# Optimization experiments

Measured on AMD Instinct MI355X. Metric: run time of the kernel, lower is better.

Reference implementation:

```python
import jax, jax.numpy as jnp
import numpy as np

B, S, E = 1, 2048, 2048
H, G, HD = 16, 4, 128  # heads, kv groups, head_dim; out_dim = H*HD = 2048
OUT_DIM = H * HD


def _rope_tables(seq_len, head_dim, base=10000.0):
    # Standard RoPE tables, full head_dim width (matches apply_rope's cos[:seq_len, :] of shape [S, HD])
    inv_freq = 1.0 / (base ** (np.arange(0, head_dim, 2, dtype=np.float32) / head_dim))
    t = np.arange(seq_len, dtype=np.float32)
    ang = np.outer(t, inv_freq)                      # [S, HD/2]
    ang = np.concatenate([ang, ang], axis=-1)        # [S, HD]
    return jnp.asarray(np.cos(ang)), jnp.asarray(np.sin(ang))


def setup_inputs() -> dict:
    key = jax.random.key(0)
    ks = jax.random.split(key, 6)
    x = jax.random.normal(ks[0], (B, S, E), dtype=jnp.float32)
    # causal mask: True above the diagonal => masked out (torch.triu(..., diagonal=1))
    mask = jnp.triu(jnp.ones((S, S), dtype=bool), k=1)
    cos, sin = _rope_tables(S, HD)
    scale = 0.02
    Wq = jax.random.normal(ks[1], (E, H * HD), dtype=jnp.float32) * scale
    Wk = jax.random.normal(ks[2], (E, G * HD), dtype=jnp.float32) * scale
    Wv = jax.random.normal(ks[3], (E, G * HD), dtype=jnp.float32) * scale
    Wout = jax.random.normal(ks[4], (H * HD, OUT_DIM), dtype=jnp.float32) * scale
    return {"x": x, "mask": mask, "cos": cos, "sin": sin,
            "Wq": Wq, "Wk": Wk, "Wv": Wv, "Wout": Wout}


def _apply_rope(t, cos, sin):
    # t: [B, h, S, HD]; cos/sin: [S, HD]
    hd = t.shape[-1]
    x1, x2 = t[..., : hd // 2], t[..., hd // 2 :]
    rotated = jnp.concatenate((-x2, x1), axis=-1)
    return t * cos[None, None] + rotated * sin[None, None]


def reference(x, mask, cos, sin, Wq, Wk, Wv, Wout):
    b, s, _ = x.shape
    q = (x @ Wq).reshape(b, s, H, HD).transpose(0, 2, 1, 3)   # [B,H,S,HD]
    k = (x @ Wk).reshape(b, s, G, HD).transpose(0, 2, 1, 3)   # [B,G,S,HD]
    v = (x @ Wv).reshape(b, s, G, HD).transpose(0, 2, 1, 3)
    q = _apply_rope(q, cos, sin)
    k = _apply_rope(k, cos, sin)
    rep = H // G
    k = jnp.repeat(k, rep, axis=1)                            # [B,H,S,HD]
    v = jnp.repeat(v, rep, axis=1)
    scores = jnp.einsum("bhqd,bhkd->bhqk", q, k)              # [B,H,S,S]
    scores = jnp.where(mask[None, None], -jnp.inf, scores)
    p = jax.nn.softmax(scores / jnp.sqrt(jnp.float32(HD)), axis=-1)
    o = jnp.einsum("bhqk,bhkd->bhqd", p, v)                   # [B,H,S,HD]
    o = o.transpose(0, 2, 1, 3).reshape(b, s, OUT_DIM)
    return (o @ Wout, p)
```

## Files before the change

### kernel.cpp

```cpp
#include <hip/hip_runtime.h>
#include <stdint.h>

#define S 2048
#define E 2048
#define NH 16
#define NG 4
#define HD 128
#define BK 64

using short8 = __attribute__((ext_vector_type(8))) short;
using f32x4  = __attribute__((ext_vector_type(4))) float;

__device__ __forceinline__ unsigned short f2bf(float f){
    union { float f; unsigned int i; } v; v.f = f;
    unsigned int x = v.i;
    unsigned int r = x + 0x7FFFu + ((x >> 16) & 1u);
    return (unsigned short)(r >> 16);
}

__device__ __forceinline__ void async_cp16(const unsigned short* g, unsigned short* l){
    __builtin_amdgcn_global_load_lds((const __attribute__((address_space(1))) void*)g,
                                     (__attribute__((address_space(3))) void*)l,
                                     16, 0, 0);
}

__device__ __forceinline__ void stage_tile_async(const unsigned short* __restrict__ G,
                                                 int ld, int k0,
                                                 unsigned short* lds)
{
    int tid = threadIdx.x;
    #pragma unroll
    for (int c = 0; c < 4; c++) {
        int e  = (c * 256 + tid) * 8;
        int r  = e >> 6;
        int cl = (e >> 3) & 7;
        int sc = cl ^ (r & 7);
        async_cp16(G + (size_t)r * ld + k0 + sc * 8, lds + e);
    }
}

__device__ __forceinline__ void stage_128x128(const unsigned short* __restrict__ G,
                                              int ld, unsigned short* lds)
{
    int tid = threadIdx.x;
    #pragma unroll
    for (int c = 0; c < 8; c++) {
        int e  = (c * 256 + tid) * 8;
        int r  = e >> 7;
        int cl = (e >> 3) & 15;
        int sc = cl ^ (r & 15);
        async_cp16(G + (size_t)r * ld + sc * 8, lds + e);
    }
}

__device__ __forceinline__ void stage_64x128(const unsigned short* __restrict__ G,
                                             int ld, unsigned short* lds)
{
    int tid = threadIdx.x;
    #pragma unroll
    for (int c = 0; c < 4; c++) {
        int e  = (c * 256 + tid) * 8;
        int r  = e >> 7;
        int cl = (e >> 3) & 15;
        int sc = cl ^ (r & 15);
        async_cp16(G + (size_t)r * ld + sc * 8, lds + e);
    }
}

__device__ __forceinline__ void gemm_core_async(const unsigned short* __restrict__ A, int lda,
                                                const unsigned short* __restrict__ Bt, int ldb,
                                                int K, f32x4 acc[4][4],
                                                unsigned short* lA, unsigned short* lB)
{
    int tid = threadIdx.x;
    int wave = tid >> 6, lane = tid & 63;
    int mBase = (wave >> 1) * 64, nBase = (wave & 1) * 64;
    int rowA = lane & 15, qc = lane >> 4;
    for (int k0 = 0; k0 < K; k0 += BK) {
        __syncthreads();
        stage_tile_async(A,  lda, k0, lA);
        stage_tile_async(Bt, ldb, k0, lB);
        __syncthreads();
        #pragma unroll
        for (int s = 0; s < 2; s++) {
            short8 af[4], bfr[4];
            #pragma unroll
            for (int i = 0; i < 4; i++) {
                int r  = mBase + i * 16 + rowA;
                int ch = (s * 4 + qc) ^ (r & 7);
                af[i] = *(const short8*)&lA[r * BK + ch * 8];
            }
            #pragma unroll
            for (int j = 0; j < 4; j++) {
                int r  = nBase + j * 16 + rowA;
                int ch = (s * 4 + qc) ^ (r & 7);
                bfr[j] = *(const short8*)&lB[r * BK + ch * 8];
            }
            #pragma unroll
            for (int i = 0; i < 4; i++)
                #pragma unroll
                for (int j = 0; j < 4; j++)
                    acc[i][j] = __builtin_amdgcn_mfma_f32_16x16x32_bf16(af[i], bfr[j], acc[i][j], 0, 0, 0);
        }
    }
}

template<bool BF16OUT>
__device__ __forceinline__ void epilogue(f32x4 acc[4][4], void* Cv, int ldc,
                                         int row0, int col0, float scale)
{
    int tid = threadIdx.x, wave = tid >> 6, lane = tid & 63;
    int mBase = (wave >> 1) * 64, nBase = (wave & 1) * 64;
    int col = lane & 15, quad = lane >> 4;
    #pragma unroll
    for (int i = 0; i < 4; i++)
        #pragma unroll
        for (int j = 0; j < 4; j++)
            #pragma unroll
            for (int r = 0; r < 4; r++) {
                int gr = row0 + mBase + i * 16 + quad * 4 + r;
                int gc = col0 + nBase + j * 16 + col;
                float v = acc[i][j][r] * scale;
                if (BF16OUT) ((unsigned short*)Cv)[(size_t)gr * ldc + gc] = f2bf(v);
                else         ((float*)Cv)[(size_t)gr * ldc + gc] = v;
            }
}

template<bool BF16OUT>
__global__ __launch_bounds__(256) void gemm_mfma_as(const unsigned short* __restrict__ A, int lda,
                                                    const unsigned short* __restrict__ Bt, int ldb,
                                                    void* __restrict__ C, int ldc, int K)
{
    __shared__ unsigned short lA[128 * BK];
    __shared__ unsigned short lB[128 * BK];
    int row0 = blockIdx.y * 128, col0 = blockIdx.x * 128;
    f32x4 acc[4][4] = {};
    gemm_core_async(A + (size_t)row0 * lda, lda, Bt + (size_t)col0 * ldb, ldb, K, acc, lA, lB);
    epilogue<BF16OUT>(acc, C, ldc, row0, col0, 1.0f);
}

__device__ __forceinline__ float rmax16(float v){
    v = fmaxf(v, __shfl_xor(v, 1)); v = fmaxf(v, __shfl_xor(v, 2));
    v = fmaxf(v, __shfl_xor(v, 4)); v = fmaxf(v, __shfl_xor(v, 8));
    return v;
}
__device__ __forceinline__ float rsum16(float v){
    v += __shfl_xor(v, 1); v += __shfl_xor(v, 2);
    v += __shfl_xor(v, 4); v += __shfl_xor(v, 8);
    return v;
}

__device__ __forceinline__ void qk_compute(const short8 qf[4], const unsigned short* lK,
                                           int rowA, int quad, f32x4 sacc[8])
{
    #pragma unroll
    for (int j = 0; j < 8; j++)
        #pragma unroll
        for (int r = 0; r < 4; r++) sacc[j][r] = 0.f;
    #pragma unroll
    for (int ks = 0; ks < 4; ks++) {
        int ch = (ks * 4 + quad) ^ rowA;
        #pragma unroll
        for (int j = 0; j < 8; j++) {
            short8 kf = *(const short8*)&lK[(j * 16 + rowA) * 128 + ch * 8];
            sacc[j] = __builtin_amdgcn_mfma_f32_16x16x32_bf16(qf[ks], kf, sacc[j], 0, 0, 0);
        }
    }
}

__global__ __launch_bounds__(256, 2) void attn_fused(const unsigned short* __restrict__ Q,
                                                     const unsigned short* __restrict__ Kb,
                                                     const unsigned short* __restrict__ Vt,
                                                     float* __restrict__ P,
                                                     unsigned short* __restrict__ Obf)
{
    __shared__ unsigned short lK[128 * 128];
    __shared__ unsigned short lV[128 * 128];
    __shared__ unsigned short lP[64 * 128];
    int h = blockIdx.x, qt = blockIdx.y, g = h >> 2;
    int jtm = qt >> 1;
    int rbase = (qt & 1) * 64;
    int tid = threadIdx.x, wave = tid >> 6, lane = tid & 63;
    int rowA = lane & 15, quad = lane >> 4;

    stage_64x128(Q + (size_t)(qt * 64) * (NH * HD) + h * HD, NH * HD, lK);
    __syncthreads();
    short8 qf[4];
    #pragma unroll
    for (int ks = 0; ks < 4; ks++) {
        int r = wave * 16 + rowA;
        int ch = (ks * 4 + quad) ^ rowA;
        qf[ks] = *(const short8*)&lK[r * 128 + ch * 8];
    }

    f32x4 m_, l_;
    #pragma unroll
    for (int r = 0; r < 4; r++) { m_[r] = -1e30f; l_[r] = 0.f; }

    for (int jt = 0; jt <= jtm; ++jt) {
        __syncthreads();
        stage_128x128(Kb + (size_t)(jt * 128) * (NG * HD) + g * HD, NG * HD, lK);
        __syncthreads();
        f32x4 sacc[8];
        qk_compute(qf, lK, rowA, quad, sacc);
        if (jt == jtm) {
            #pragma unroll
            for (int j = 0; j < 8; j++)
                #pragma unroll
                for (int r = 0; r < 4; r++) {
                    int row = rbase + wave * 16 + quad * 4 + r;
                    int col = j * 16 + rowA;
                    if (col > row) sacc[j][r] = -1e30f;
                }
        }
        #pragma unroll
        for (int r = 0; r < 4; r++) {
            float tm = sacc[0][r];
            #pragma unroll
            for (int j = 1; j < 8; j++) tm = fmaxf(tm, sacc[j][r]);
            tm = rmax16(tm);
            float mn = fmaxf(m_[r], tm);
            float es = 0.f;
            #pragma unroll
            for (int j = 0; j < 8; j++) es += __expf(sacc[j][r] - mn);
            es = rsum16(es);
            l_[r] = l_[r] * __expf(m_[r] - mn) + es;
            m_[r] = mn;
        }
    }
    f32x4 linv;
    #pragma unroll
    for (int r = 0; r < 4; r++) linv[r] = 1.0f / l_[r];

    f32x4 oacc[8];
    #pragma unroll
    for (int j = 0; j < 8; j++)
        #pragma unroll
        for (int r = 0; r < 4; r++) oacc[j][r] = 0.f;

    for (int jt = 0; jt <= jtm; ++jt) {
        __syncthreads();
        stage_128x128(Kb + (size_t)(jt * 128) * (NG * HD) + g * HD, NG * HD, lK);
        stage_128x128(Vt + (size_t)(g * HD) * S + jt * 128, S, lV);
        __syncthreads();
        f32x4 sacc[8];
        qk_compute(qf, lK, rowA, quad, sacc);
        if (jt == jtm) {
            #pragma unroll
            for (int j = 0; j < 8; j++)
                #pragma unroll
                for (int r = 0; r < 4; r++) {
                    int row = rbase + wave * 16 + quad * 4 + r;
                    int col = j * 16 + rowA;
                    if (col > row) sacc[j][r] = -1e30f;
                }
        }
        float* Prow = P + ((size_t)h * S + qt * 64) * S + jt * 128;
        #pragma unroll
        for (int j = 0; j < 8; j++)
            #pragma unroll
            for (int r = 0; r < 4; r++) {
                int row = wave * 16 + quad * 4 + r;
                int col = j * 16 + rowA;
                float pv = __expf(sacc[j][r] - m_[r]) * linv[r];
                Prow[(size_t)row * S + col] = pv;
                int ch = col >> 3;
                lP[row * 128 + (((ch ^ (row & 15)) << 3) | (col & 7))] = f2bf(pv);
            }
        __syncthreads();
        #pragma unroll
        for (int ks = 0; ks < 4; ks++) {
            int ch = (ks * 4 + quad) ^ rowA;
            short8 pa = *(const short8*)&lP[(wave * 16 + rowA) * 128 + ch * 8];
            #pragma unroll
            for (int j = 0; j < 8; j++) {
                short8 vb = *(const short8*)&lV[(j * 16 + rowA) * 128 + ch * 8];
                oacc[j] = __builtin_amdgcn_mfma_f32_16x16x32_bf16(pa, vb, oacc[j], 0, 0, 0);
            }
        }
    }

    #pragma unroll
    for (int j = 0; j < 8; j++)
        #pragma unroll
        for (int r = 0; r < 4; r++) {
            int row = qt * 64 + wave * 16 + quad * 4 + r;
            int col = h * HD + j * 16 + rowA;
            Obf[(size_t)row * (NH * HD) + col] = f2bf(oacc[j][r]);
        }

    int zc0 = (jtm + 1) * 128;
    float* Pz = P + ((size_t)h * S + qt * 64) * S;
    for (int rr = 0; rr < 64; ++rr)
        for (int c = zc0 + tid * 4; c < S; c += 1024)
            *(float4*)(Pz + (size_t)rr * S + c) = make_float4(0.f, 0.f, 0.f, 0.f);
}

__global__ __launch_bounds__(256) void transpose_cvt(const float* __restrict__ in,
                                                     unsigned short* __restrict__ out,
                                                     int R, int C, int inLd)
{
    __shared__ float t[32][33];
    int r0 = blockIdx.y * 32, c0 = blockIdx.x * 32;
    int tid = threadIdx.x;
    int rr = tid >> 3, cc = (tid & 7) * 4;
    float4 v = *(const float4*)(in + (size_t)(r0 + rr) * inLd + c0 + cc);
    t[rr][cc] = v.x; t[rr][cc + 1] = v.y; t[rr][cc + 2] = v.z; t[rr][cc + 3] = v.w;
    __syncthreads();
    int oc = tid >> 3, orr = (tid & 7) * 4;
    ushort4 o;
    o.x = f2bf(t[orr][oc]);     o.y = f2bf(t[orr + 1][oc]);
    o.z = f2bf(t[orr + 2][oc]); o.w = f2bf(t[orr + 3][oc]);
    *(ushort4*)(out + (size_t)(c0 + oc) * R + r0 + orr) = o;
}

__global__ __launch_bounds__(256) void cvt_bf16(const float* __restrict__ in,
                                                unsigned short* __restrict__ out, int n)
{
    int i = (blockIdx.x * 256 + threadIdx.x) * 8;
    if (i >= n) return;
    float4 a = *(const float4*)(in + i);
    float4 b = *(const float4*)(in + i + 4);
    unsigned int w0 = (unsigned int)f2bf(a.x) | ((unsigned int)f2bf(a.y) << 16);
    unsigned int w1 = (unsigned int)f2bf(a.z) | ((unsigned int)f2bf(a.w) << 16);
    unsigned int w2 = (unsigned int)f2bf(b.x) | ((unsigned int)f2bf(b.y) << 16);
    unsigned int w3 = (unsigned int)f2bf(b.z) | ((unsigned int)f2bf(b.w) << 16);
    *(uint4*)(out + i) = make_uint4(w0, w1, w2, w3);
}

__global__ void rope_bf16(const float* __restrict__ T, unsigned short* __restrict__ Tb,
                          const float* __restrict__ cosp, const float* __restrict__ sinp,
                          int nHeads, int inLd, int inOff, int outLd, float scale, int total)
{
    int idx = blockIdx.x * blockDim.x + threadIdx.x;
    if (idx >= total) return;
    int d = idx & 63;
    int head = (idx >> 6) % nHeads;
    int s = idx / (nHeads * 64);
    float c  = cosp[s * HD + d];
    float sn = sinp[s * HD + d];
    const float* ib = T + (size_t)s * inLd + inOff + head * HD + d;
    float x1 = ib[0], x2 = ib[64];
    unsigned short* ob = Tb + (size_t)s * outLd + head * HD + d;
    ob[0]  = f2bf((x1 * c - x2 * sn) * scale);
    ob[64] = f2bf((x2 * c + x1 * sn) * scale);
}

extern "C" void kernel_launch(void* const* d_in, const int* in_sizes, int n_in,
                              void* d_out, int out_size, void* d_ws, size_t ws_size,
                              hipStream_t stream)
{
    const float* x    = (const float*)d_in[0];
    const float* cosp = (const float*)d_in[2];
    const float* sinp = (const float*)d_in[3];
    const float* Wq   = (const float*)d_in[4];
    const float* Wk   = (const float*)d_in[5];
    const float* Wv   = (const float*)d_in[6];
    const float* Wout = (const float*)d_in[7];

    float* out0 = (float*)d_out;
    float* Pout = out0 + (size_t)S * E;

    unsigned short* Wqkvt = (unsigned short*)d_ws;
    unsigned short* Qbf   = Wqkvt + (size_t)3072 * E;
    unsigned short* Kbf   = Qbf   + (size_t)S * E;
    unsigned short* Vt    = Kbf   + (size_t)S * (NG * HD);
    unsigned short* Obf   = Vt    + (size_t)(NG * HD) * S;
    float* QKVb = (float*)(Obf + (size_t)S * E);
    unsigned short* xbf   = Obf;
    unsigned short* Woutt = (unsigned short*)QKVb;

    dim3 blk(256);
    transpose_cvt<<<dim3(E / 32, E / 32), blk, 0, stream>>>(Wq, Wqkvt, E, E, E);
    transpose_cvt<<<dim3((NG * HD) / 32, E / 32), blk, 0, stream>>>(Wk, Wqkvt + (size_t)E * E, E, NG * HD, NG * HD);
    transpose_cvt<<<dim3((NG * HD) / 32, E / 32), blk, 0, stream>>>(Wv, Wqkvt + (size_t)(E + NG * HD) * E, E, NG * HD, NG * HD);
    cvt_bf16<<<dim3((S * E) / (256 * 8)), blk, 0, stream>>>(x, xbf, S * E);

    gemm_mfma_as<false><<<dim3(3072 / 128, S / 128), blk, 0, stream>>>(xbf, E, Wqkvt, E, QKVb, 3072, E);

    rope_bf16<<<(S * NH * 64 + 255) / 256, blk, 0, stream>>>(QKVb, Qbf, cosp, sinp, NH, 3072, 0, NH * HD,
                                                             0.08838834764831845f, S * NH * 64);
    rope_bf16<<<(S * NG * 64 + 255) / 256, blk, 0, stream>>>(QKVb, Kbf, cosp, sinp, NG, 3072, E, NG * HD,
                                                             1.0f, S * NG * 64);
    transpose_cvt<<<dim3((NG * HD) / 32, S / 32), blk, 0, stream>>>(QKVb + E + NG * HD, Vt, S, NG * HD, 3072);

    transpose_cvt<<<dim3(E / 32, E / 32), blk, 0, stream>>>(Wout, Woutt, E, E, E);

    attn_fused<<<dim3(NH, S / 64), blk, 0, stream>>>(Qbf, Kbf, Vt, Pout, Obf);

    gemm_mfma_as<false><<<dim3(E / 128, S / 128), blk, 0, stream>>>(Obf, E, Woutt, E, out0, E, E);
}
```

Before: 498.9 us.

## Split attention into single-pass flash kernel plus separate tiled P writer

Replaces the two-pass attention (a stats pass, then recompute and write P) with a one-pass online-softmax flash kernel that saves only the row max and inverse sum. A new p_write kernel recomputes QK^T per 128x128 tile using those stats and writes the normalized probabilities or zeros with coalesced, well-parallelized stores. The GEMM core also gains double-buffered LDS staging to overlap loads with MFMA, and attention blocks are launched in reverse order so the longest causal rows start first. This costs an extra QK^T recompute and doubles GEMM shared memory.

```diff
diff --git a/kernel.cpp b/kernel.cpp
--- a/kernel.cpp
+++ b/kernel.cpp
@@ -76,11 +76,18 @@
     int wave = tid >> 6, lane = tid & 63;
     int mBase = (wave >> 1) * 64, nBase = (wave & 1) * 64;
     int rowA = lane & 15, qc = lane >> 4;
-    for (int k0 = 0; k0 < K; k0 += BK) {
-        __syncthreads();
-        stage_tile_async(A,  lda, k0, lA);
-        stage_tile_async(Bt, ldb, k0, lB);
-        __syncthreads();
+    int nt = K / BK;
+    stage_tile_async(A,  lda, 0, lA);
+    stage_tile_async(Bt, ldb, 0, lB);
+    __syncthreads();
+    int cur = 0;
+    for (int t = 0; t < nt; ++t) {
+        if (t + 1 < nt) {
+            stage_tile_async(A,  lda, (t + 1) * BK, lA + (cur ^ 1) * (128 * BK));
+            stage_tile_async(Bt, ldb, (t + 1) * BK, lB + (cur ^ 1) * (128 * BK));
+        }
+        const unsigned short* cA = lA + cur * (128 * BK);
+        const unsigned short* cB = lB + cur * (128 * BK);
         #pragma unroll
         for (int s = 0; s < 2; s++) {
             short8 af[4], bfr[4];
@@ -88,13 +95,13 @@
             for (int i = 0; i < 4; i++) {
                 int r  = mBase + i * 16 + rowA;
                 int ch = (s * 4 + qc) ^ (r & 7);
-                af[i] = *(const short8*)&lA[r * BK + ch * 8];
+                af[i] = *(const short8*)&cA[r * BK + ch * 8];
             }
             #pragma unroll
             for (int j = 0; j < 4; j++) {
                 int r  = nBase + j * 16 + rowA;
                 int ch = (s * 4 + qc) ^ (r & 7);
-                bfr[j] = *(const short8*)&lB[r * BK + ch * 8];
+                bfr[j] = *(const short8*)&cB[r * BK + ch * 8];
             }
             #pragma unroll
             for (int i = 0; i < 4; i++)
@@ -102,6 +109,8 @@
                 for (int j = 0; j < 4; j++)
                     acc[i][j] = __builtin_amdgcn_mfma_f32_16x16x32_bf16(af[i], bfr[j], acc[i][j], 0, 0, 0);
         }
+        __syncthreads();
+        cur ^= 1;
     }
 }
 
@@ -131,8 +140,8 @@
                                                     const unsigned short* __restrict__ Bt, int ldb,
                                                     void* __restrict__ C, int ldc, int K)
 {
-    __shared__ unsigned short lA[128 * BK];
-    __shared__ unsigned short lB[128 * BK];
+    __shared__ unsigned short lA[2 * 128 * BK];
+    __shared__ unsigned short lB[2 * 128 * BK];
     int row0 = blockIdx.y * 128, col0 = blockIdx.x * 128;
     f32x4 acc[4][4] = {};
     gemm_core_async(A + (size_t)row0 * lda, lda, Bt + (size_t)col0 * ldb, ldb, K, acc, lA, lB);
@@ -168,16 +177,17 @@
     }
 }
 
-__global__ __launch_bounds__(256, 2) void attn_fused(const unsigned short* __restrict__ Q,
+__global__ __launch_bounds__(256, 2) void attn_flash(const unsigned short* __restrict__ Q,
                                                      const unsigned short* __restrict__ Kb,
                                                      const unsigned short* __restrict__ Vt,
-                                                     float* __restrict__ P,
-                                                     unsigned short* __restrict__ Obf)
+                                                     unsigned short* __restrict__ Obf,
+                                                     float* __restrict__ Mrow,
+                                                     float* __restrict__ Li)
 {
     __shared__ unsigned short lK[128 * 128];
     __shared__ unsigned short lV[128 * 128];
     __shared__ unsigned short lP[64 * 128];
-    int h = blockIdx.x, qt = blockIdx.y, g = h >> 2;
+    int h = blockIdx.x, qt = (gridDim.y - 1) - blockIdx.y, g = h >> 2;
     int jtm = qt >> 1;
     int rbase = (qt & 1) * 64;
     int tid = threadIdx.x, wave = tid >> 6, lane = tid & 63;
@@ -196,42 +206,6 @@
     f32x4 m_, l_;
     #pragma unroll
     for (int r = 0; r < 4; r++) { m_[r] = -1e30f; l_[r] = 0.f; }
-
-    for (int jt = 0; jt <= jtm; ++jt) {
-        __syncthreads();
-        stage_128x128(Kb + (size_t)(jt * 128) * (NG * HD) + g * HD, NG * HD, lK);
-        __syncthreads();
-        f32x4 sacc[8];
-        qk_compute(qf, lK, rowA, quad, sacc);
-        if (jt == jtm) {
-            #pragma unroll
-            for (int j = 0; j < 8; j++)
-                #pragma unroll
-                for (int r = 0; r < 4; r++) {
-                    int row = rbase + wave * 16 + quad * 4 + r;
-                    int col = j * 16 + rowA;
-                    if (col > row) sacc[j][r] = -1e30f;
-                }
-        }
-        #pragma unroll
-        for (int r = 0; r < 4; r++) {
-            float tm = sacc[0][r];
-            #pragma unroll
-            for (int j = 1; j < 8; j++) tm = fmaxf(tm, sacc[j][r]);
-            tm = rmax16(tm);
-            float mn = fmaxf(m_[r], tm);
-            float es = 0.f;
-            #pragma unroll
-            for (int j = 0; j < 8; j++) es += __expf(sacc[j][r] - mn);
-            es = rsum16(es);
-            l_[r] = l_[r] * __expf(m_[r] - mn) + es;
-            m_[r] = mn;
-        }
-    }
-    f32x4 linv;
-    #pragma unroll
-    for (int r = 0; r < 4; r++) linv[r] = 1.0f / l_[r];
-
     f32x4 oacc[8];
     #pragma unroll
     for (int j = 0; j < 8; j++)
@@ -255,17 +229,35 @@
                     if (col > row) sacc[j][r] = -1e30f;
                 }
         }
-        float* Prow = P + ((size_t)h * S + qt * 64) * S + jt * 128;
+        #pragma unroll
+        for (int r = 0; r < 4; r++) {
+            float tm = sacc[0][r];
+            #pragma unroll
+            for (int j = 1; j < 8; j++) tm = fmaxf(tm, sacc[j][r]);
+            tm = rmax16(tm);
+            float mn = fmaxf(m_[r], tm);
+            float sc = __expf(m_[r] - mn);
+            float es = 0.f;
+            #pragma unroll
+            for (int j = 0; j < 8; j++) {
+                float p = __expf(sacc[j][r] - mn);
+                sacc[j][r] = p;
+                es += p;
+            }
+            es = rsum16(es);
+            l_[r] = l_[r] * sc + es;
+            m_[r] = mn;
+            #pragma unroll
+            for (int j = 0; j < 8; j++) oacc[j][r] *= sc;
+        }
         #pragma unroll
         for (int j = 0; j < 8; j++)
             #pragma unroll
             for (int r = 0; r < 4; r++) {
                 int row = wave * 16 + quad * 4 + r;
                 int col = j * 16 + rowA;
-                float pv = __expf(sacc[j][r] - m_[r]) * linv[r];
-                Prow[(size_t)row * S + col] = pv;
                 int ch = col >> 3;
-                lP[row * 128 + (((ch ^ (row & 15)) << 3) | (col & 7))] = f2bf(pv);
+                lP[row * 128 + (((ch ^ (row & 15)) << 3) | (col & 7))] = f2bf(sacc[j][r]);
             }
         __syncthreads();
         #pragma unroll
@@ -280,20 +272,78 @@
         }
     }
 
+    f32x4 linv;
+    #pragma unroll
+    for (int r = 0; r < 4; r++) linv[r] = 1.0f / l_[r];
+
     #pragma unroll
     for (int j = 0; j < 8; j++)
         #pragma unroll
         for (int r = 0; r < 4; r++) {
             int row = qt * 64 + wave * 16 + quad * 4 + r;
             int col = h * HD + j * 16 + rowA;
-            Obf[(size_t)row * (NH * HD) + col] = f2bf(oacc[j][r]);
-        }
-
-    int zc0 = (jtm + 1) * 128;
-    float* Pz = P + ((size_t)h * S + qt * 64) * S;
-    for (int rr = 0; rr < 64; ++rr)
-        for (int c = zc0 + tid * 4; c < S; c += 1024)
-            *(float4*)(Pz + (size_t)rr * S + c) = make_float4(0.f, 0.f, 0.f, 0.f);
+            Obf[(size_t)row * (NH * HD) + col] = f2bf(oacc[j][r] * linv[r]);
+        }
+
+    if (rowA == 0) {
+        int grow0 = qt * 64 + wave * 16 + quad * 4;
+        #pragma unroll
+        for (int r = 0; r < 4; r++) {
+            Mrow[(size_t)h * S + grow0 + r] = m_[r];
+            Li[(size_t)h * S + grow0 + r]  = linv[r];
+        }
+    }
+}
+
+__global__ __launch_bounds__(256) void p_write(const unsigned short* __restrict__ Q,
+                                               const unsigned short* __restrict__ Kb,
+                                               const float* __restrict__ Mrow,
+                                               const float* __restrict__ Li,
+                                               float* __restrict__ P)
+{
+    int jt = blockIdx.x, it = blockIdx.y, h = blockIdx.z;
+    float* Pt = P + (size_t)h * S * S + (size_t)(it * 128) * S + jt * 128;
+    int tid = threadIdx.x;
+    if (jt > it) {
+        #pragma unroll
+        for (int q = 0; q < 16; q++) {
+            int e4 = q * 256 + tid;
+            int r  = e4 >> 5;
+            int c4 = (e4 & 31) * 4;
+            *(float4*)(Pt + (size_t)r * S + c4) = make_float4(0.f, 0.f, 0.f, 0.f);
+        }
+        return;
+    }
+    __shared__ unsigned short lA[2 * 128 * BK];
+    __shared__ unsigned short lB[2 * 128 * BK];
+    f32x4 acc[4][4] = {};
+    gemm_core_async(Q + (size_t)(it * 128) * (NH * HD) + h * HD, NH * HD,
+                    Kb + (size_t)(jt * 128) * (NG * HD) + (h >> 2) * HD, NG * HD,
+                    HD, acc, lA, lB);
+    int wave = tid >> 6, lane = tid & 63;
+    int mBase = (wave >> 1) * 64, nBase = (wave & 1) * 64;
+    int col = lane & 15, quad = lane >> 4;
+    bool diag = (jt == it);
+    #pragma unroll
+    for (int i = 0; i < 4; i++) {
+        float mm[4], li[4];
+        #pragma unroll
+        for (int r = 0; r < 4; r++) {
+            int gr = it * 128 + mBase + i * 16 + quad * 4 + r;
+            mm[r] = Mrow[(size_t)h * S + gr];
+            li[r] = Li[(size_t)h * S + gr];
+        }
+        #pragma unroll
+        for (int j = 0; j < 4; j++)
+            #pragma unroll
+            for (int r = 0; r < 4; r++) {
+                int lr = mBase + i * 16 + quad * 4 + r;
+                int lc = nBase + j * 16 + col;
+                float v = (diag && lc > lr) ? 0.f
+                          : __expf(acc[i][j][r] - mm[r]) * li[r];
+                Pt[(size_t)lr * S + lc] = v;
+            }
+    }
 }
 
 __global__ __launch_bounds__(256) void transpose_cvt(const float* __restrict__ in,
@@ -367,6 +417,8 @@
     unsigned short* Vt    = Kbf   + (size_t)S * (NG * HD);
     unsigned short* Obf   = Vt    + (size_t)(NG * HD) * S;
     float* QKVb = (float*)(Obf + (size_t)S * E);
+    float* Mrow = QKVb + (size_t)S * 3072;
+    float* Li   = Mrow + (size_t)NH * S;
     unsigned short* xbf   = Obf;
     unsigned short* Woutt = (unsigned short*)QKVb;
 
@@ -386,7 +438,9 @@
 
     transpose_cvt<<<dim3(E / 32, E / 32), blk, 0, stream>>>(Wout, Woutt, E, E, E);
 
-    attn_fused<<<dim3(NH, S / 64), blk, 0, stream>>>(Qbf, Kbf, Vt, Pout, Obf);
+    attn_flash<<<dim3(NH, S / 64), blk, 0, stream>>>(Qbf, Kbf, Vt, Obf, Mrow, Li);
+
+    p_write<<<dim3(S / 128, S / 128, NH), blk, 0, stream>>>(Qbf, Kbf, Mrow, Li, Pout);
 
     gemm_mfma_as<false><<<dim3(E / 128, S / 128), blk, 0, stream>>>(Obf, E, Woutt, E, out0, E, E);
 }
```

Result: no change. 490.5 us, median of 2 (-1.7%).
